# Performance work log

Hardware: AMD Instinct MI355X
Metric: run time of the kernel (lower is better)

## Reference

```python
import jax, jax.numpy as jnp
import numpy as np
import math

B, T, C, H, D = 4, 2048, 1024, 16, 64  # batch, seq, n_embd, n_head, head_dim


def setup_inputs() -> dict:
    key = jax.random.key(0)
    kx, kq, kk, kv, ko = jax.random.split(key, 5)
    x = jax.random.normal(kx, (B, T, C), dtype=jnp.float32)
    # standard RoPE tables, half head_dim
    d = D // 2
    inv_freq = 1.0 / (10000.0 ** (jnp.arange(d, dtype=jnp.float32) / d))
    freqs = jnp.outer(jnp.arange(T, dtype=jnp.float32), inv_freq)  # [T, d]
    cos = jnp.cos(freqs)[None, None]  # [1,1,T,d]
    sin = jnp.sin(freqs)[None, None]
    s = 0.02
    Wq = jax.random.normal(kq, (C, C), dtype=jnp.float32) * s  # stored [in,out]
    Wk = jax.random.normal(kk, (C, C), dtype=jnp.float32) * s
    Wv = jax.random.normal(kv, (C, C), dtype=jnp.float32) * s
    Wo = jax.random.normal(ko, (C, C), dtype=jnp.float32) * s
    return {"x": x, "cos": cos, "sin": sin, "Wq": Wq, "Wk": Wk, "Wv": Wv, "Wo": Wo}


def _rope(u, cos, sin):
    # u: [B,H,T,D]; rotate-half style RoPE matching apply_rotary_emb
    d = u.shape[-1] // 2
    u1, u2 = u[..., :d], u[..., d:]
    return jnp.concatenate([u1 * cos + u2 * sin, -u1 * sin + u2 * cos], axis=-1)


def _rms_norm(u):
    # parameter-free RMSNorm, eps = finfo eps (torch F.rms_norm default)
    eps = jnp.finfo(u.dtype).eps
    return u * jax.lax.rsqrt(jnp.mean(u * u, axis=-1, keepdims=True) + eps)


def reference(x, cos, sin, Wq, Wk, Wv, Wo):
    b, t, c = x.shape

    def split_heads(h):
        return h.reshape(b, t, H, D).transpose(0, 2, 1, 3)  # [B,H,T,D]

    q = split_heads(x @ Wq)
    k = split_heads(x @ Wk)
    v = split_heads(x @ Wv)
    q = _rms_norm(_rope(q, cos, sin))
    k = _rms_norm(_rope(k, cos, sin))
    scale = 1.0 / math.sqrt(D)
    scores = jnp.einsum('bhqd,bhkd->bhqk', q, k) * scale  # [B,H,T,T]
    causal = jnp.tril(jnp.ones((t, t), dtype=bool))
    scores = jnp.where(causal, scores, -jnp.inf)
    attn = jax.nn.softmax(scores, axis=-1)
    y = jnp.einsum('bhqk,bhkd->bhqd', attn, v)
    y = y.transpose(0, 2, 1, 3).reshape(b, t, c)
    return y @ Wo
```

## Files before the change

### kernel.cpp

```cpp
#include <hip/hip_runtime.h>


typedef __attribute__((ext_vector_type(8))) short short8;
typedef __attribute__((ext_vector_type(4))) short short4v;
typedef __attribute__((ext_vector_type(4))) float f32x4;

__device__ __forceinline__ unsigned short f2b(float f) {
  union { float f; unsigned int i; } x; x.f = f;
  return (unsigned short)((x.i + 0x7FFFu + ((x.i >> 16) & 1u)) >> 16);
}

__device__ __forceinline__ unsigned short b16(float f) {
  return __builtin_bit_cast(unsigned short, (__bf16)f);
}

__device__ __forceinline__ void glds16(const void* g, void* l) {
  __builtin_amdgcn_global_load_lds((const __attribute__((address_space(1))) unsigned int*)g,
                                   (__attribute__((address_space(3))) unsigned int*)l,
                                   16, 0, 0);
}

__device__ __forceinline__ f32x4 mfma16(short8 a, short8 b, f32x4 c) {
  return __builtin_amdgcn_mfma_f32_16x16x32_bf16(a, b, c, 0, 0, 0);
}

__global__ __launch_bounds__(256) void prep_kernel(
    const float* __restrict__ x, unsigned short* __restrict__ xb,
    const float* __restrict__ W0, const float* __restrict__ W1,
    const float* __restrict__ W2, const float* __restrict__ W3,
    unsigned short* __restrict__ Wt, unsigned short* __restrict__ Wot) {
  const int z = blockIdx.z;
  if (z >= 4) {
    const long blk = (long)(z - 4) * 1024 + blockIdx.y * 32 + blockIdx.x;
    const long i = (blk * 256 + threadIdx.x) * 8;
    const float4 a = *(const float4*)(x + i);
    const float4 b = *(const float4*)(x + i + 4);
    unsigned short o[8] = {f2b(a.x), f2b(a.y), f2b(a.z), f2b(a.w),
                           f2b(b.x), f2b(b.y), f2b(b.z), f2b(b.w)};
    *(short8*)(xb + i) = *(const short8*)o;
    return;
  }
  const float* __restrict__ W = (z == 0) ? W0 : (z == 1) ? W1 : (z == 2) ? W2 : W3;
  unsigned short* __restrict__ dst = (z < 3) ? (Wt + (size_t)z * 1024 * 1024) : Wot;
  __shared__ float tile[32][33];
  const int tx = threadIdx.x & 31, ty = threadIdx.x >> 5;
  const int bx = blockIdx.x * 32, by = blockIdx.y * 32;
#pragma unroll
  for (int i = 0; i < 4; ++i)
    tile[ty + 8 * i][tx] = W[(size_t)(by + ty + 8 * i) * 1024 + bx + tx];
  __syncthreads();
#pragma unroll
  for (int i = 0; i < 4; ++i)
    dst[(size_t)(bx + ty + 8 * i) * 1024 + by + tx] = f2b(tile[tx][ty + 8 * i]);
}

__global__ __launch_bounds__(256) void gemm_qkv(
    const unsigned short* __restrict__ A, const unsigned short* __restrict__ Bt,
    unsigned short* __restrict__ Qr, unsigned short* __restrict__ Kr,
    unsigned short* __restrict__ Vr,
    const float* __restrict__ cosp, const float* __restrict__ sinp) {
  __shared__ unsigned short As[128 * 64];
  __shared__ unsigned short Bs[128 * 64];
  const int tid = threadIdx.x;
  const int wave = tid >> 6, lane = tid & 63;
  const int ln = lane & 15, grp = lane >> 4;
  const int wr = wave >> 1, wc = wave & 1;
  const int row0 = blockIdx.x * 128, col0 = blockIdx.y * 128;

  f32x4 acc[4][4];
  const f32x4 z4 = {0.f, 0.f, 0.f, 0.f};
#pragma unroll
  for (int m = 0; m < 4; ++m)
#pragma unroll
    for (int n = 0; n < 4; ++n) acc[m][n] = z4;

  const int sw = (ln & 7) << 4;

  for (int k0 = 0; k0 < 1024; k0 += 64) {
    __syncthreads();
#pragma unroll
    for (int it = 0; it < 4; ++it) {
      const int cl = it * 256 + tid;
      const int r = cl >> 3;
      const int sc = ((cl & 7) ^ (r & 7)) * 8;
      glds16(A + (long)(row0 + r) * 1024 + k0 + sc, (char*)As + it * 4096 + wave * 1024);
      glds16(Bt + (long)(col0 + r) * 1024 + k0 + sc, (char*)Bs + it * 4096 + wave * 1024);
    }
    __syncthreads();
#pragma unroll
    for (int ks = 0; ks < 2; ++ks) {
      short8 af[4], bfv[4];
#pragma unroll
      for (int m = 0; m < 4; ++m) {
        const int row = wr * 64 + m * 16 + ln;
        af[m] = *(const short8*)((const char*)As + row * 128 + ((grp * 16 + ks * 64) ^ sw));
      }
#pragma unroll
      for (int n = 0; n < 4; ++n) {
        const int row = wc * 64 + n * 16 + ln;
        bfv[n] = *(const short8*)((const char*)Bs + row * 128 + ((grp * 16 + ks * 64) ^ sw));
      }
#pragma unroll
      for (int m = 0; m < 4; ++m)
#pragma unroll
        for (int n = 0; n < 4; ++n)
          acc[m][n] = mfma16(af[m], bfv[n], acc[m][n]);
    }
  }

  const int colbase = col0 + wc * 64;
  const int z = colbase >> 10;
  const int h = (colbase & 1023) >> 6;
  unsigned short* __restrict__ dst = (z == 0) ? Qr : (z == 1) ? Kr : Vr;

  if (z < 2) {
    const float qs = (z == 0) ? 0.125f * 1.44269504f : 1.0f;
#pragma unroll
    for (int m = 0; m < 4; ++m) {
#pragma unroll
      for (int reg = 0; reg < 4; ++reg) {
        const int row = row0 + wr * 64 + m * 16 + grp * 4 + reg;
        const int t = row & 2047, b = row >> 11;
        const float u0 = acc[m][0][reg], u1 = acc[m][1][reg];
        const float u2 = acc[m][2][reg], u3 = acc[m][3][reg];
        const float c0 = cosp[t * 32 + ln],      s0 = sinp[t * 32 + ln];
        const float c1 = cosp[t * 32 + 16 + ln], s1 = sinp[t * 32 + 16 + ln];
        const float r0 =  u0 * c0 + u2 * s0;
        const float r1 =  u1 * c1 + u3 * s1;
        const float r2 = -u0 * s0 + u2 * c0;
        const float r3 = -u1 * s1 + u3 * c1;
        float ss = r0 * r0 + r1 * r1 + r2 * r2 + r3 * r3;
        ss += __shfl_xor(ss, 1); ss += __shfl_xor(ss, 2);
        ss += __shfl_xor(ss, 4); ss += __shfl_xor(ss, 8);
        const float inv = rsqrtf(ss * (1.0f / 64.0f) + 1.1920929e-07f) * qs;
        const long base = (((long)(b * 16 + h)) * 2048 + t) * 64;
        dst[base + ln]      = f2b(r0 * inv);
        dst[base + 16 + ln] = f2b(r1 * inv);
        dst[base + 32 + ln] = f2b(r2 * inv);
        dst[base + 48 + ln] = f2b(r3 * inv);
      }
    }
  } else {
#pragma unroll
    for (int m = 0; m < 4; ++m) {
#pragma unroll
      for (int reg = 0; reg < 4; ++reg) {
        const int row = row0 + wr * 64 + m * 16 + grp * 4 + reg;
        const int t = row & 2047, b = row >> 11;
        const long base = (((long)(b * 16 + h)) * 2048 + t) * 64;
#pragma unroll
        for (int n = 0; n < 4; ++n)
          dst[base + n * 16 + ln] = f2b(acc[m][n][reg]);
      }
    }
  }
}

__global__ __launch_bounds__(256) void attn_kernel(
    const unsigned short* __restrict__ Q, const unsigned short* __restrict__ K,
    const unsigned short* __restrict__ V, unsigned short* __restrict__ Y) {
  __shared__ unsigned short lds[2 * 8192];
  const int tid = threadIdx.x;
  const int wave = tid >> 6, lane = tid & 63;
  const int ln = lane & 15, grp = lane >> 4;

  const int linb = blockIdx.x;
  const int xcd = linb & 7, slot = linb >> 3;
  const int bh = xcd * 8 + (slot >> 4);
  const int pr = slot & 15;

  const long bhT = (long)bh * 2048;
  const int b = bh >> 4, h = bh & 15;
  auto* lds3 = (__attribute__((address_space(3))) unsigned short*)lds;

  const short o1 = (short)0x3f80;
  const short8 ones = {o1, o1, o1, o1, o1, o1, o1, o1};

  auto stage = [&](int j, int buf) {
    const long kvoff = bhT + (long)j * 64;
    char* Kb = (char*)lds + buf * 16384;
#pragma unroll
    for (int p = 0; p < 2; ++p) {
      const int cl = p * 256 + tid;
      const int krow = cl >> 3;
      const int kcb = ((cl & 7) * 16) ^ ((krow & 7) << 4);
      glds16(K + (kvoff + krow) * 64 + (kcb >> 1), Kb + p * 4096 + wave * 1024);
      const int dtv = cl >> 7, kvt = (cl >> 3) & 15, rr = (cl >> 1) & 3, hf = cl & 1;
      glds16(V + (kvoff + kvt * 4 + rr) * 64 + dtv * 16 + hf * 8,
             Kb + 8192 + p * 4096 + wave * 1024);
    }
  };

  const f32x4 z4 = {0.f, 0.f, 0.f, 0.f};

  for (int half = 0; half < 2; ++half) {
    const int bx = (half == 0) ? pr : 31 - pr;
    const int qw = bx * 64 + wave * 16;
    const int jmax = bx;

    short8 qf[2];
#pragma unroll
    for (int c = 0; c < 2; ++c)
      qf[c] = *(const short8*)(Q + (bhT + qw + ln) * 64 + c * 32 + grp * 8);

    f32x4 accO[4];
#pragma unroll
    for (int dt = 0; dt < 4; ++dt) accO[dt] = z4;
    f32x4 accL = z4;

    stage(0, 0);
    asm volatile("s_waitcnt vmcnt(0)" ::: "memory");
    __builtin_amdgcn_s_barrier();

    int cur = 0;
    for (int j = 0; j <= jmax; ++j, cur ^= 1) {
      if (j < jmax) {
        stage(j + 1, cur ^ 1);
        asm volatile("s_waitcnt vmcnt(4)" ::: "memory");
      } else {
        asm volatile("s_waitcnt vmcnt(0)" ::: "memory");
      }
      __builtin_amdgcn_s_barrier();

      const unsigned short* Kb = lds + cur * 8192;
      const bool maskp = (j == jmax);

      f32x4 sacc[4];
#pragma unroll
      for (int ct = 0; ct < 4; ++ct) sacc[ct] = z4;
      __builtin_amdgcn_s_setprio(1);
#pragma unroll
      for (int ct = 0; ct < 4; ++ct) {
        const int row = ct * 16 + ln;
        const int sw = (ln & 7) << 4;
        const char* rp = (const char*)Kb + row * 128;
        const short8 kf0 = *(const short8*)(rp + ((grp * 16) ^ sw));
        const short8 kf1 = *(const short8*)(rp + ((grp * 16 + 64) ^ sw));
        sacc[ct] = mfma16(kf0, qf[0], sacc[ct]);
        sacc[ct] = mfma16(kf1, qf[1], sacc[ct]);
      }
      __builtin_amdgcn_s_setprio(0);

      short8 pf[2];
      {
        if (maskp) {
          const int q = qw + ln;
#pragma unroll
          for (int ct = 0; ct < 4; ++ct)
#pragma unroll
            for (int r = 0; r < 4; ++r) {
              const int kv = j * 64 + ct * 16 + grp * 4 + r;
              if (kv > q) sacc[ct][r] = -INFINITY;
            }
        }
#pragma unroll
        for (int ct = 0; ct < 4; ++ct)
#pragma unroll
          for (int r = 0; r < 4; ++r)
            pf[ct >> 1][(ct & 1) * 4 + r] = (short)b16(exp2f(sacc[ct][r]));
      }

      const unsigned vb = (unsigned)(size_t)&lds3[cur * 8192 + 4096] + (unsigned)lane * 8;
      short4v t[4][4];
#pragma unroll
      for (int dt = 0; dt < 4; ++dt) {
        const unsigned va = vb + dt * 2048;
        asm volatile("ds_read_b64_tr_b16 %0, %4 offset:0\n\t"
                     "ds_read_b64_tr_b16 %1, %4 offset:512\n\t"
                     "ds_read_b64_tr_b16 %2, %4 offset:1024\n\t"
                     "ds_read_b64_tr_b16 %3, %4 offset:1536"
                     : "=&v"(t[dt][0]), "=&v"(t[dt][1]), "=&v"(t[dt][2]), "=&v"(t[dt][3])
                     : "v"(va));
      }
      asm volatile("s_waitcnt lgkmcnt(0)" ::: "memory");
      __builtin_amdgcn_sched_barrier(0);
      __builtin_amdgcn_s_setprio(1);
#pragma unroll
      for (int dt = 0; dt < 4; ++dt) {
        const short8 vf0 = __builtin_shufflevector(t[dt][0], t[dt][1], 0, 1, 2, 3, 4, 5, 6, 7);
        const short8 vf1 = __builtin_shufflevector(t[dt][2], t[dt][3], 0, 1, 2, 3, 4, 5, 6, 7);
        accO[dt] = mfma16(vf0, pf[0], accO[dt]);
        accO[dt] = mfma16(vf1, pf[1], accO[dt]);
      }
      accL = mfma16(ones, pf[0], accL);
      accL = mfma16(ones, pf[1], accL);
      __builtin_amdgcn_s_setprio(0);
      __builtin_amdgcn_s_barrier();
    }

    {
      const float inv = 1.0f / accL[0];
      const int t_ = qw + ln;
      const long base = (((long)(b * 2048 + t_)) * 16 + h) * 64;
#pragma unroll
      for (int dt = 0; dt < 4; ++dt) {
        unsigned short o[4];
#pragma unroll
        for (int r = 0; r < 4; ++r) o[r] = b16(accO[dt][r] * inv);
        *(short4v*)(Y + base + dt * 16 + grp * 4) = *(const short4v*)o;
      }
    }
  }
}

__global__ __launch_bounds__(256) void gemm_out(
    const unsigned short* __restrict__ A, const unsigned short* __restrict__ Bt,
    float* __restrict__ C) {
  __shared__ unsigned short As[128 * 64];
  __shared__ unsigned short Bs[128 * 64];
  const int tid = threadIdx.x;
  const int wave = tid >> 6, lane = tid & 63;
  const int ln = lane & 15, grp = lane >> 4;
  const int wr = wave >> 1, wc = wave & 1;
  const int row0 = blockIdx.x * 128, col0 = blockIdx.y * 128;

  f32x4 acc[4][4];
  const f32x4 z4 = {0.f, 0.f, 0.f, 0.f};
#pragma unroll
  for (int m = 0; m < 4; ++m)
#pragma unroll
    for (int n = 0; n < 4; ++n) acc[m][n] = z4;

  const int sw = (ln & 7) << 4;

  for (int k0 = 0; k0 < 1024; k0 += 64) {
    __syncthreads();
#pragma unroll
    for (int it = 0; it < 4; ++it) {
      const int cl = it * 256 + tid;
      const int r = cl >> 3;
      const int sc = ((cl & 7) ^ (r & 7)) * 8;
      glds16(A + (long)(row0 + r) * 1024 + k0 + sc, (char*)As + it * 4096 + wave * 1024);
      glds16(Bt + (long)(col0 + r) * 1024 + k0 + sc, (char*)Bs + it * 4096 + wave * 1024);
    }
    __syncthreads();
#pragma unroll
    for (int ks = 0; ks < 2; ++ks) {
      short8 af[4], bfv[4];
#pragma unroll
      for (int m = 0; m < 4; ++m) {
        const int row = wr * 64 + m * 16 + ln;
        af[m] = *(const short8*)((const char*)As + row * 128 + ((grp * 16 + ks * 64) ^ sw));
      }
#pragma unroll
      for (int n = 0; n < 4; ++n) {
        const int row = wc * 64 + n * 16 + ln;
        bfv[n] = *(const short8*)((const char*)Bs + row * 128 + ((grp * 16 + ks * 64) ^ sw));
      }
#pragma unroll
      for (int m = 0; m < 4; ++m)
#pragma unroll
        for (int n = 0; n < 4; ++n)
          acc[m][n] = mfma16(af[m], bfv[n], acc[m][n]);
    }
  }

#pragma unroll
  for (int m = 0; m < 4; ++m)
#pragma unroll
    for (int reg = 0; reg < 4; ++reg) {
      const int row = row0 + wr * 64 + m * 16 + grp * 4 + reg;
#pragma unroll
      for (int n = 0; n < 4; ++n)
        C[(long)row * 1024 + col0 + wc * 64 + n * 16 + ln] = acc[m][n][reg];
    }
}

extern "C" void kernel_launch(void* const* d_in, const int* in_sizes, int n_in,
                              void* d_out, int out_size, void* d_ws, size_t ws_size,
                              hipStream_t stream) {
  (void)in_sizes; (void)n_in; (void)out_size; (void)ws_size;
  const float* x    = (const float*)d_in[0];
  const float* cosp = (const float*)d_in[1];
  const float* sinp = (const float*)d_in[2];
  const float* Wq   = (const float*)d_in[3];
  const float* Wk   = (const float*)d_in[4];
  const float* Wv   = (const float*)d_in[5];
  const float* Wo   = (const float*)d_in[6];
  float* out = (float*)d_out;

  unsigned short* xb  = (unsigned short*)d_ws;
  unsigned short* Wt  = xb  + (size_t)8192 * 1024;
  unsigned short* Wot = Wt  + (size_t)3 * 1024 * 1024;
  unsigned short* Qr  = Wot + (size_t)1024 * 1024;
  unsigned short* Kr  = Qr  + (size_t)8192 * 1024;
  unsigned short* Vr  = Kr  + (size_t)8192 * 1024;
  unsigned short* Yb  = xb;

  prep_kernel<<<dim3(32, 32, 8), 256, 0, stream>>>(x, xb, Wq, Wk, Wv, Wo, Wt, Wot);
  gemm_qkv<<<dim3(64, 24), 256, 0, stream>>>(xb, Wt, Qr, Kr, Vr, cosp, sinp);
  attn_kernel<<<1024, 256, 0, stream>>>(Qr, Kr, Vr, Yb);
  gemm_out<<<dim3(64, 8), 256, 0, stream>>>(Yb, Wot, out);
}
```

Baseline: 178.1 us.

## Process 128 query rows per attention block to double K/V tile reuse

Each wave now owns two 16-row query tiles (32 rows), so each block covers a 128-row query tile. Every staged K/V LDS tile feeds twice as many MFMAs, and there are half as many barriers and staging rounds per unit of work. The causal mask now applies to the last two KV tiles. The paired short/long 64-row halves are replaced by one tile per block, with a bit-permuted tile order meant to spread long and short blocks across the grid. The V transposed reads now wait per dt chunk instead of all at once. In exchange, register pressure goes up and load balancing is coarser.

```diff
diff --git a/kernel.cpp b/kernel.cpp
--- a/kernel.cpp
+++ b/kernel.cpp
@@ -166,8 +166,10 @@
 
   const int linb = blockIdx.x;
   const int xcd = linb & 7, slot = linb >> 3;
-  const int bh = xcd * 8 + (slot >> 4);
-  const int pr = slot & 15;
+  const int bh = xcd * 8 + (slot & 7);
+  const int u = slot >> 3;
+  const int r3 = ((u & 1) << 2) | (u & 2) | ((u >> 2) & 1);
+  const int bx = (u & 8) ? r3 : 15 - r3;
 
   const long bhT = (long)bh * 2048;
   const int b = bh >> 4, h = bh & 15;
@@ -193,112 +195,117 @@
 
   const f32x4 z4 = {0.f, 0.f, 0.f, 0.f};
 
-  for (int half = 0; half < 2; ++half) {
-    const int bx = (half == 0) ? pr : 31 - pr;
-    const int qw = bx * 64 + wave * 16;
-    const int jmax = bx;
-
-    short8 qf[2];
+  const int qw = bx * 128 + wave * 32;
+  const int jmax = 2 * bx + 1;
+  const int jdiag = 2 * bx;
+
+  short8 qf[2][2];
+#pragma unroll
+  for (int nt = 0; nt < 2; ++nt)
 #pragma unroll
     for (int c = 0; c < 2; ++c)
-      qf[c] = *(const short8*)(Q + (bhT + qw + ln) * 64 + c * 32 + grp * 8);
-
-    f32x4 accO[4];
-#pragma unroll
-    for (int dt = 0; dt < 4; ++dt) accO[dt] = z4;
-    f32x4 accL = z4;
-
-    stage(0, 0);
-    asm volatile("s_waitcnt vmcnt(0)" ::: "memory");
+      qf[nt][c] = *(const short8*)(Q + (bhT + qw + nt * 16 + ln) * 64 + c * 32 + grp * 8);
+
+  f32x4 accO[4][2];
+#pragma unroll
+  for (int dt = 0; dt < 4; ++dt) { accO[dt][0] = z4; accO[dt][1] = z4; }
+  f32x4 accL[2] = {z4, z4};
+
+  stage(0, 0);
+  asm volatile("s_waitcnt vmcnt(0)" ::: "memory");
+  __builtin_amdgcn_s_barrier();
+
+  int cur = 0;
+  for (int j = 0; j <= jmax; ++j, cur ^= 1) {
+    if (j < jmax) {
+      stage(j + 1, cur ^ 1);
+      asm volatile("s_waitcnt vmcnt(4)" ::: "memory");
+    } else {
+      asm volatile("s_waitcnt vmcnt(0)" ::: "memory");
+    }
     __builtin_amdgcn_s_barrier();
 
-    int cur = 0;
-    for (int j = 0; j <= jmax; ++j, cur ^= 1) {
-      if (j < jmax) {
-        stage(j + 1, cur ^ 1);
-        asm volatile("s_waitcnt vmcnt(4)" ::: "memory");
-      } else {
-        asm volatile("s_waitcnt vmcnt(0)" ::: "memory");
-      }
-      __builtin_amdgcn_s_barrier();
-
-      const unsigned short* Kb = lds + cur * 8192;
-      const bool maskp = (j == jmax);
-
-      f32x4 sacc[4];
-#pragma unroll
-      for (int ct = 0; ct < 4; ++ct) sacc[ct] = z4;
-      __builtin_amdgcn_s_setprio(1);
-#pragma unroll
-      for (int ct = 0; ct < 4; ++ct) {
-        const int row = ct * 16 + ln;
-        const int sw = (ln & 7) << 4;
-        const char* rp = (const char*)Kb + row * 128;
-        const short8 kf0 = *(const short8*)(rp + ((grp * 16) ^ sw));
-        const short8 kf1 = *(const short8*)(rp + ((grp * 16 + 64) ^ sw));
-        sacc[ct] = mfma16(kf0, qf[0], sacc[ct]);
-        sacc[ct] = mfma16(kf1, qf[1], sacc[ct]);
-      }
-      __builtin_amdgcn_s_setprio(0);
-
-      short8 pf[2];
-      {
-        if (maskp) {
-          const int q = qw + ln;
-#pragma unroll
-          for (int ct = 0; ct < 4; ++ct)
-#pragma unroll
-            for (int r = 0; r < 4; ++r) {
-              const int kv = j * 64 + ct * 16 + grp * 4 + r;
-              if (kv > q) sacc[ct][r] = -INFINITY;
-            }
-        }
+    const unsigned short* Kb = lds + cur * 8192;
+    const bool maskp = (j >= jdiag);
+
+    f32x4 sacc[4][2];
+#pragma unroll
+    for (int ct = 0; ct < 4; ++ct) { sacc[ct][0] = z4; sacc[ct][1] = z4; }
+    __builtin_amdgcn_s_setprio(1);
+#pragma unroll
+    for (int ct = 0; ct < 4; ++ct) {
+      const int row = ct * 16 + ln;
+      const int sw = (ln & 7) << 4;
+      const char* rp = (const char*)Kb + row * 128;
+      const short8 kf0 = *(const short8*)(rp + ((grp * 16) ^ sw));
+      const short8 kf1 = *(const short8*)(rp + ((grp * 16 + 64) ^ sw));
+      sacc[ct][0] = mfma16(kf0, qf[0][0], sacc[ct][0]);
+      sacc[ct][0] = mfma16(kf1, qf[0][1], sacc[ct][0]);
+      sacc[ct][1] = mfma16(kf0, qf[1][0], sacc[ct][1]);
+      sacc[ct][1] = mfma16(kf1, qf[1][1], sacc[ct][1]);
+    }
+    __builtin_amdgcn_s_setprio(0);
+
+    short8 pf[2][2];
+#pragma unroll
+    for (int nt = 0; nt < 2; ++nt) {
+      if (maskp) {
+        const int q = qw + nt * 16 + ln;
 #pragma unroll
         for (int ct = 0; ct < 4; ++ct)
 #pragma unroll
-          for (int r = 0; r < 4; ++r)
-            pf[ct >> 1][(ct & 1) * 4 + r] = (short)b16(exp2f(sacc[ct][r]));
-      }
-
-      const unsigned vb = (unsigned)(size_t)&lds3[cur * 8192 + 4096] + (unsigned)lane * 8;
-      short4v t[4][4];
-#pragma unroll
-      for (int dt = 0; dt < 4; ++dt) {
-        const unsigned va = vb + dt * 2048;
-        asm volatile("ds_read_b64_tr_b16 %0, %4 offset:0\n\t"
-                     "ds_read_b64_tr_b16 %1, %4 offset:512\n\t"
-                     "ds_read_b64_tr_b16 %2, %4 offset:1024\n\t"
-                     "ds_read_b64_tr_b16 %3, %4 offset:1536"
-                     : "=&v"(t[dt][0]), "=&v"(t[dt][1]), "=&v"(t[dt][2]), "=&v"(t[dt][3])
-                     : "v"(va));
-      }
+          for (int r = 0; r < 4; ++r) {
+            const int kv = j * 64 + ct * 16 + grp * 4 + r;
+            if (kv > q) sacc[ct][nt][r] = -INFINITY;
+          }
+      }
+#pragma unroll
+      for (int ct = 0; ct < 4; ++ct)
+#pragma unroll
+        for (int r = 0; r < 4; ++r)
+          pf[nt][ct >> 1][(ct & 1) * 4 + r] = (short)b16(exp2f(sacc[ct][nt][r]));
+    }
+
+    const unsigned vb = (unsigned)(size_t)&lds3[cur * 8192 + 4096] + (unsigned)lane * 8;
+    __builtin_amdgcn_s_setprio(1);
+#pragma unroll
+    for (int dt = 0; dt < 4; ++dt) {
+      const unsigned va = vb + dt * 2048;
+      short4v t0, t1, t2, t3;
+      asm volatile("ds_read_b64_tr_b16 %0, %4 offset:0\n\t"
+                   "ds_read_b64_tr_b16 %1, %4 offset:512\n\t"
+                   "ds_read_b64_tr_b16 %2, %4 offset:1024\n\t"
+                   "ds_read_b64_tr_b16 %3, %4 offset:1536"
+                   : "=&v"(t0), "=&v"(t1), "=&v"(t2), "=&v"(t3)
+                   : "v"(va));
       asm volatile("s_waitcnt lgkmcnt(0)" ::: "memory");
       __builtin_amdgcn_sched_barrier(0);
-      __builtin_amdgcn_s_setprio(1);
-#pragma unroll
-      for (int dt = 0; dt < 4; ++dt) {
-        const short8 vf0 = __builtin_shufflevector(t[dt][0], t[dt][1], 0, 1, 2, 3, 4, 5, 6, 7);
-        const short8 vf1 = __builtin_shufflevector(t[dt][2], t[dt][3], 0, 1, 2, 3, 4, 5, 6, 7);
-        accO[dt] = mfma16(vf0, pf[0], accO[dt]);
-        accO[dt] = mfma16(vf1, pf[1], accO[dt]);
-      }
-      accL = mfma16(ones, pf[0], accL);
-      accL = mfma16(ones, pf[1], accL);
-      __builtin_amdgcn_s_setprio(0);
-      __builtin_amdgcn_s_barrier();
-    }
-
-    {
-      const float inv = 1.0f / accL[0];
-      const int t_ = qw + ln;
-      const long base = (((long)(b * 2048 + t_)) * 16 + h) * 64;
-#pragma unroll
-      for (int dt = 0; dt < 4; ++dt) {
-        unsigned short o[4];
-#pragma unroll
-        for (int r = 0; r < 4; ++r) o[r] = b16(accO[dt][r] * inv);
-        *(short4v*)(Y + base + dt * 16 + grp * 4) = *(const short4v*)o;
-      }
+      const short8 vf0 = __builtin_shufflevector(t0, t1, 0, 1, 2, 3, 4, 5, 6, 7);
+      const short8 vf1 = __builtin_shufflevector(t2, t3, 0, 1, 2, 3, 4, 5, 6, 7);
+      accO[dt][0] = mfma16(vf0, pf[0][0], accO[dt][0]);
+      accO[dt][0] = mfma16(vf1, pf[0][1], accO[dt][0]);
+      accO[dt][1] = mfma16(vf0, pf[1][0], accO[dt][1]);
+      accO[dt][1] = mfma16(vf1, pf[1][1], accO[dt][1]);
+    }
+    accL[0] = mfma16(ones, pf[0][0], accL[0]);
+    accL[0] = mfma16(ones, pf[0][1], accL[0]);
+    accL[1] = mfma16(ones, pf[1][0], accL[1]);
+    accL[1] = mfma16(ones, pf[1][1], accL[1]);
+    __builtin_amdgcn_s_setprio(0);
+    __builtin_amdgcn_s_barrier();
+  }
+
+#pragma unroll
+  for (int nt = 0; nt < 2; ++nt) {
+    const float inv = 1.0f / accL[nt][0];
+    const int t_ = qw + nt * 16 + ln;
+    const long base = (((long)(b * 2048 + t_)) * 16 + h) * 64;
+#pragma unroll
+    for (int dt = 0; dt < 4; ++dt) {
+      unsigned short o[4];
+#pragma unroll
+      for (int r = 0; r < 4; ++r) o[r] = b16(accO[dt][nt][r] * inv);
+      *(short4v*)(Y + base + dt * 16 + grp * 4) = *(const short4v*)o;
     }
   }
 }
```

Result: slower. 187.0 us (+5.0%).
